# Kernel optimization log

Hardware: AMD Instinct MI355X
Metric: run time of the kernel (lower is better)

## Reference

```python
import jax, jax.numpy as jnp
import numpy as np

N, E, F_IN, D, L = 100000, 1600000, 32, 128, 5
B, V, T, EMB = 3000, 64, 128, 64
H = L * D  # 640 LSTM hidden
BN_EPS = 1e-5


def setup_inputs():
    key = jax.random.key(0)
    ks = jax.random.split(key, 20)
    rn = lambda k, s, sc=0.05: jax.random.normal(k, s, jnp.float32) * sc
    inp = {
        'x': jax.random.normal(ks[0], (N, F_IN), jnp.float32),
        'edge_index': jax.random.randint(ks[1], (2, E), 0, N, jnp.int32),
        'batch': jnp.sort(jax.random.randint(ks[2], (N,), 0, B, jnp.int32)),
        'smi': jax.random.randint(ks[3], (B, T), 0, V, jnp.int32),
        'gin0_w1': rn(ks[4], (F_IN, D)), 'gin0_b1': jnp.zeros((D,), jnp.float32),
        'gin0_w2': rn(ks[5], (D, D)),    'gin0_b2': jnp.zeros((D,), jnp.float32),
        'ginr_w1': rn(ks[6], (L - 1, D, D)), 'ginr_b1': jnp.zeros((L - 1, D), jnp.float32),
        'ginr_w2': rn(ks[7], (L - 1, D, D)), 'ginr_b2': jnp.zeros((L - 1, D), jnp.float32),
        'bn_gamma': jnp.ones((L, D), jnp.float32), 'bn_beta': jnp.zeros((L, D), jnp.float32),
        'emb': rn(ks[8], (V, EMB), 0.1).at[0].set(0.0),  # padding_idx=0
        'w_ih': rn(ks[9], (4 * H, EMB), 0.04), 'w_hh': rn(ks[10], (4 * H, H), 0.04),
        'b_ih': jnp.zeros((4 * H,), jnp.float32), 'b_hh': jnp.zeros((4 * H,), jnp.float32),
        'g_w1': rn(ks[11], (L * D, 4 * D)), 'g_b1': jnp.zeros((4 * D,), jnp.float32),
        'g_bn_gamma': jnp.ones((4 * D,), jnp.float32), 'g_bn_beta': jnp.zeros((4 * D,), jnp.float32),
        'g_w2': rn(ks[12], (4 * D, 6 * D)),
    }
    return inp


def _bn(h, gamma, beta):
    # BatchNorm1d in training mode: biased batch statistics
    mu = h.mean(0)
    var = h.var(0)
    return (h - mu) * jax.lax.rsqrt(var + BN_EPS) * gamma + beta


def _gin_layer(h, src, dst, w1, b1, w2, b2, gamma, beta):
    # GINConv (eps=0): MLP(x + sum_{j->i} x_j), then ReLU, then BN
    agg = jax.ops.segment_sum(h[src], dst, num_segments=N)  # [N, d]
    z = h + agg
    z = jnp.maximum(z @ w1 + b1, 0.0) @ w2 + b2
    z = jnp.maximum(z, 0.0)
    return _bn(z, gamma, beta)


def _lstm_last(e, w_ih, w_hh, b_ih, b_hh):
    # e: [B, T, EMB] -> last hidden state [B, H]
    def step(carry, xt):
        h, c = carry
        gates = xt @ w_ih.T + b_ih + h @ w_hh.T + b_hh  # [B, 4H]
        i, f, g, o = jnp.split(gates, 4, axis=1)  # torch gate order i,f,g,o
        c = jax.nn.sigmoid(f) * c + jax.nn.sigmoid(i) * jnp.tanh(g)
        h = jax.nn.sigmoid(o) * jnp.tanh(c)
        return (h, c), None
    h0 = jnp.zeros((e.shape[0], H), e.dtype)
    (h, _), _ = jax.lax.scan(step, (h0, h0), e.transpose(1, 0, 2))
    return h


def reference(x, edge_index, batch, smi, gin0_w1, gin0_b1, gin0_w2, gin0_b2,
              ginr_w1, ginr_b1, ginr_w2, ginr_b2, bn_gamma, bn_beta, emb,
              w_ih, w_hh, b_ih, b_hh, g_w1, g_b1, g_bn_gamma, g_bn_beta, g_w2):
    src, dst = edge_index[0], edge_index[1]
    # --- GIN encoder with layer-wise global_add_pool ---
    h = _gin_layer(x, src, dst, gin0_w1, gin0_b1, gin0_w2, gin0_b2, bn_gamma[0], bn_beta[0])
    pools = [jax.ops.segment_sum(h, batch, num_segments=B)]
    for i in range(L - 1):
        h = _gin_layer(h, src, dst, ginr_w1[i], ginr_b1[i], ginr_w2[i], ginr_b2[i],
                       bn_gamma[i + 1], bn_beta[i + 1])
        pools.append(jax.ops.segment_sum(h, batch, num_segments=B))
    enc1 = jnp.concatenate(pools, axis=1)  # [B, L*D]
    # --- SMILES encoder: Embedding + LSTM, take output at last timestep ---
    enc2 = _lstm_last(emb[smi], w_ih, w_hh, b_ih, b_hh)  # [B, H] == [B, L*D]
    # --- shared projection head g, L2-normalized (F.normalize, eps=1e-12) ---
    def g_head(z):
        z1 = jnp.maximum(_bn(z @ g_w1 + g_b1, g_bn_gamma, g_bn_beta), 0.0)
        out = z1 @ g_w2
        nrm = jnp.maximum(jnp.linalg.norm(out, axis=1, keepdims=True), 1e-12)
        return out / nrm
    return (g_head(enc1), g_head(enc2))
```

## Files before the change

### kernel.cpp

```cpp
#include <hip/hip_runtime.h>

typedef __bf16 bf16x8 __attribute__((ext_vector_type(8)));
typedef float f32x4 __attribute__((ext_vector_type(4)));
typedef unsigned short ushort8 __attribute__((ext_vector_type(8)));

#define DEV static __device__ __forceinline__

DEV unsigned short f2bf(float f){
  unsigned int u = __builtin_bit_cast(unsigned int, f);
  u += 0x7fffu + ((u >> 16) & 1u);
  return (unsigned short)(u >> 16);
}
DEV float bf2f(unsigned short u){
  return __builtin_bit_cast(float, ((unsigned int)u) << 16);
}
DEV float sigf(float x){ return 1.0f/(1.0f + __expf(-x)); }

static constexpr int NN   = 100000;
static constexpr int NPAD = 100096;
static constexpr int NE   = 1600000;
static constexpr int NB   = 3000;
static constexpr int BPAD = 3072;
static constexpr int TT   = 128;
static constexpr int HID  = 640;
static constexpr int SCAN_B = 1024;
static constexpr int NBLK = (NN + SCAN_B - 1)/SCAN_B;

__global__ void cvt_k(const float* __restrict__ s, unsigned short* __restrict__ d, int n){
  int i = blockIdx.x*256 + threadIdx.x; if (i < n) d[i] = f2bf(s[i]);
}
__global__ void transpose_cvt_split_k(const float* __restrict__ s, unsigned short* __restrict__ dh,
                                      unsigned short* __restrict__ dl, int R, int C){
  int i = blockIdx.x*256 + threadIdx.x; if (i >= R*C) return;
  int r = i / C, c = i - r*C;
  float v = s[i];
  unsigned short hi = f2bf(v);
  dh[c*R + r] = hi;
  dl[c*R + r] = f2bf(v - bf2f(hi));
}
__global__ void wc2_build_k(const float* __restrict__ whh, const float* __restrict__ wih,
                            unsigned short* __restrict__ wc2){
  int i = blockIdx.x*256 + threadIdx.x; if (i >= 2560*704) return;
  int n2 = i / 704, k = i - n2*704;
  int jt = n2 >> 7, rem = n2 & 127;
  int hc = rem >> 6, gate = (rem >> 4) & 3, j15 = rem & 15;
  int n = gate*640 + jt*32 + hc*16 + j15;
  float v = (k < 640) ? whh[n*640 + k] : wih[n*64 + (k - 640)];
  wc2[i] = f2bf(v);
}
__global__ void add_k(const float* __restrict__ a, const float* __restrict__ b, float* __restrict__ o, int n){
  int i = blockIdx.x*256 + threadIdx.x; if (i < n) o[i] = a[i] + b[i];
}

__global__ __launch_bounds__(256) void deg_hist_k(const int* __restrict__ dsts, int* __restrict__ deg){
  int e = blockIdx.x*256 + threadIdx.x; if (e < NE) atomicAdd(&deg[dsts[e]], 1);
}
__global__ __launch_bounds__(256) void scan_bsum_k(const int* __restrict__ deg, int* __restrict__ bsum){
  __shared__ int red[4];
  int b = blockIdx.x, tid = threadIdx.x;
  int base = b*SCAN_B + tid*4;
  int s = 0;
  #pragma unroll
  for (int q = 0; q < 4; ++q){ int idx = base + q; s += (idx < NN) ? deg[idx] : 0; }
  #pragma unroll
  for (int m = 1; m < 64; m <<= 1) s += __shfl_xor(s, m);
  if ((tid & 63) == 0) red[tid >> 6] = s;
  __syncthreads();
  if (tid == 0) bsum[b] = red[0] + red[1] + red[2] + red[3];
}
__global__ void scan_off_k(int* __restrict__ bsum){
  if (threadIdx.x == 0){
    int run = 0;
    for (int i = 0; i < NBLK; ++i){ int t = bsum[i]; bsum[i] = run; run += t; }
  }
}
__global__ __launch_bounds__(256) void scan_write_k(const int* __restrict__ deg, const int* __restrict__ bsum,
                                                    int* __restrict__ rowptr, int* __restrict__ cursor){
  __shared__ int tsum[256];
  int b = blockIdx.x, tid = threadIdx.x;
  int base = b*SCAN_B + tid*4;
  int v[4]; int s = 0;
  #pragma unroll
  for (int q = 0; q < 4; ++q){ int idx = base + q; v[q] = (idx < NN) ? deg[idx] : 0; s += v[q]; }
  tsum[tid] = s;
  __syncthreads();
  for (int offt = 1; offt < 256; offt <<= 1){
    int y = (tid >= offt) ? tsum[tid - offt] : 0;
    __syncthreads();
    tsum[tid] += y;
    __syncthreads();
  }
  int run = bsum[b] + tsum[tid] - s;
  #pragma unroll
  for (int q = 0; q < 4; ++q){
    int idx = base + q;
    if (idx < NN){ rowptr[idx] = run; cursor[idx] = run; }
    run += v[q];
  }
  if (b == 0 && tid == 0) rowptr[NN] = NE;
}
__global__ __launch_bounds__(256) void csr_fill_k(const int* __restrict__ srcs, const int* __restrict__ dsts,
                                                  int* __restrict__ cursor, int* __restrict__ eidx){
  int e = blockIdx.x*256 + threadIdx.x; if (e >= NE) return;
  int d = dsts[e];
  int pos = atomicAdd(&cursor[d], 1);
  eidx[pos] = srcs[e];
}

__global__ __launch_bounds__(256) void gbound_k(const int* __restrict__ batch, int* __restrict__ gstart){
  int i = blockIdx.x*256 + threadIdx.x;
  if (i >= NN) return;
  int bi = batch[i];
  int bp = (i == 0) ? -1 : batch[i-1];
  for (int g = bp + 1; g <= bi; ++g) gstart[g] = i;
  if (i == NN-1){
    for (int g = bi + 1; g <= NB; ++g) gstart[g] = NN;
  }
}

__global__ __launch_bounds__(256) void agg128_k(const int* __restrict__ rowptr, const int* __restrict__ eidx,
    const float* __restrict__ H, float* __restrict__ Z){
  int wid = (blockIdx.x*256 + threadIdx.x) >> 6;
  if (wid >= NN) return;
  int lane = threadIdx.x & 63;
  const float2* Hp = (const float2*)H;
  int n0 = rowptr[wid], n1 = rowptr[wid+1];
  float2 acc = Hp[(size_t)wid*64 + lane];
  int i = n0;
  for (; i + 1 < n1; i += 2){
    int s0 = eidx[i], s1 = eidx[i+1];
    float2 v0 = Hp[(size_t)s0*64 + lane];
    float2 v1 = Hp[(size_t)s1*64 + lane];
    acc.x += v0.x + v1.x; acc.y += v0.y + v1.y;
  }
  if (i < n1){
    float2 v = Hp[(size_t)eidx[i]*64 + lane];
    acc.x += v.x; acc.y += v.y;
  }
  ((float2*)Z)[(size_t)wid*64 + lane] = acc;
}
__global__ __launch_bounds__(256) void agg32_k(const int* __restrict__ rowptr, const int* __restrict__ eidx,
    const float* __restrict__ X, float* __restrict__ Z){
  int r = (blockIdx.x*256 + threadIdx.x) >> 5;
  if (r >= NN) return;
  int l = threadIdx.x & 31;
  int n0 = rowptr[r], n1 = rowptr[r+1];
  float acc = X[(size_t)r*32 + l];
  int i = n0;
  for (; i + 1 < n1; i += 2){
    int s0 = eidx[i], s1 = eidx[i+1];
    acc += X[(size_t)s0*32 + l] + X[(size_t)s1*32 + l];
  }
  if (i < n1) acc += X[(size_t)eidx[i]*32 + l];
  Z[(size_t)r*32 + l] = acc;
}

template<int KIN>
__global__ __launch_bounds__(256) void gin_mlp_k(const float* __restrict__ Z,
    const unsigned short* __restrict__ W1h, const unsigned short* __restrict__ W1l,
    const unsigned short* __restrict__ W2h, const unsigned short* __restrict__ W2l,
    const float* __restrict__ b1, const float* __restrict__ b2,
    float* __restrict__ Y, float* __restrict__ stats)
{
  constexpr int SA = KIN + 8;
  __shared__ __align__(16) unsigned short Ah[128*136];
  __shared__ __align__(16) unsigned short Al[128*136];
  const int tid = threadIdx.x, lane = tid & 63, w = tid >> 6;
  const int row0 = blockIdx.x * 128;
  const int wr = (w >> 1)*64, wc0 = (w & 1)*64;
  const int l15 = lane & 15, lg = lane >> 4;

  constexpr int CH = KIN/8;
  #pragma unroll
  for (int i = 0; i < (128*CH)/256; ++i){
    int chunk = tid + 256*i;
    int row = chunk / CH, kc = (chunk - row*CH)*8;
    const float* sp = Z + (size_t)(row0 + row)*KIN + kc;
    float4 a0 = *(const float4*)sp;
    float4 a1 = *(const float4*)(sp + 4);
    float vv[8] = {a0.x,a0.y,a0.z,a0.w,a1.x,a1.y,a1.z,a1.w};
    ushort8 vh, vl;
    #pragma unroll
    for (int q=0;q<8;++q){ unsigned short h = f2bf(vv[q]); vh[q]=h; vl[q]=f2bf(vv[q]-bf2f(h)); }
    *(ushort8*)&Ah[row*SA + kc] = vh;
    *(ushort8*)&Al[row*SA + kc] = vl;
  }
  __syncthreads();

  f32x4 acc[4][4];
  #pragma unroll
  for (int i=0;i<4;++i)
    #pragma unroll
    for (int j=0;j<4;++j) acc[i][j] = (f32x4)(0.0f);

  #pragma unroll
  for (int k0 = 0; k0 < KIN; k0 += 32){
    bf16x8 ah[4], al[4], bh[4], bl[4];
    #pragma unroll
    for (int fa=0; fa<4; ++fa){
      ah[fa] = *(const bf16x8*)&Ah[(wr + fa*16 + l15)*SA + k0 + 8*lg];
      al[fa] = *(const bf16x8*)&Al[(wr + fa*16 + l15)*SA + k0 + 8*lg];
    }
    #pragma unroll
    for (int fb=0; fb<4; ++fb){
      bh[fb] = *(const bf16x8*)&W1h[(wc0 + fb*16 + l15)*KIN + k0 + 8*lg];
      bl[fb] = *(const bf16x8*)&W1l[(wc0 + fb*16 + l15)*KIN + k0 + 8*lg];
    }
    #pragma unroll
    for (int fa=0; fa<4; ++fa)
      #pragma unroll
      for (int fb=0; fb<4; ++fb){
        acc[fa][fb] = __builtin_amdgcn_mfma_f32_16x16x32_bf16(ah[fa], bh[fb], acc[fa][fb], 0, 0, 0);
        acc[fa][fb] = __builtin_amdgcn_mfma_f32_16x16x32_bf16(al[fa], bh[fb], acc[fa][fb], 0, 0, 0);
        acc[fa][fb] = __builtin_amdgcn_mfma_f32_16x16x32_bf16(ah[fa], bl[fb], acc[fa][fb], 0, 0, 0);
      }
  }
  __syncthreads();

  {
    float b1v[4];
    #pragma unroll
    for (int fb=0; fb<4; ++fb) b1v[fb] = b1[wc0 + fb*16 + l15];
    #pragma unroll
    for (int fa=0; fa<4; ++fa)
      #pragma unroll
      for (int fb=0; fb<4; ++fb)
        #pragma unroll
        for (int r=0; r<4; ++r){
          float v = fmaxf(acc[fa][fb][r] + b1v[fb], 0.0f);
          unsigned short h = f2bf(v);
          int idx = (wr + fa*16 + lg*4 + r)*136 + (wc0 + fb*16 + l15);
          Ah[idx] = h;
          Al[idx] = f2bf(v - bf2f(h));
        }
  }
  __syncthreads();

  f32x4 acc2[4][4];
  #pragma unroll
  for (int i=0;i<4;++i)
    #pragma unroll
    for (int j=0;j<4;++j) acc2[i][j] = (f32x4)(0.0f);

  #pragma unroll
  for (int k0 = 0; k0 < 128; k0 += 32){
    bf16x8 ah[4], al[4], bh[4], bl[4];
    #pragma unroll
    for (int fa=0; fa<4; ++fa){
      ah[fa] = *(const bf16x8*)&Ah[(wr + fa*16 + l15)*136 + k0 + 8*lg];
      al[fa] = *(const bf16x8*)&Al[(wr + fa*16 + l15)*136 + k0 + 8*lg];
    }
    #pragma unroll
    for (int fb=0; fb<4; ++fb){
      bh[fb] = *(const bf16x8*)&W2h[(wc0 + fb*16 + l15)*128 + k0 + 8*lg];
      bl[fb] = *(const bf16x8*)&W2l[(wc0 + fb*16 + l15)*128 + k0 + 8*lg];
    }
    #pragma unroll
    for (int fa=0; fa<4; ++fa)
      #pragma unroll
      for (int fb=0; fb<4; ++fb){
        acc2[fa][fb] = __builtin_amdgcn_mfma_f32_16x16x32_bf16(ah[fa], bh[fb], acc2[fa][fb], 0, 0, 0);
        acc2[fa][fb] = __builtin_amdgcn_mfma_f32_16x16x32_bf16(al[fa], bh[fb], acc2[fa][fb], 0, 0, 0);
        acc2[fa][fb] = __builtin_amdgcn_mfma_f32_16x16x32_bf16(ah[fa], bl[fb], acc2[fa][fb], 0, 0, 0);
      }
  }

  float b2v[4]; int cc[4];
  #pragma unroll
  for (int fb=0; fb<4; ++fb){ cc[fb] = wc0 + fb*16 + l15; b2v[fb] = b2[cc[fb]]; }
  float ps[4] = {0,0,0,0}, pq[4] = {0,0,0,0};
  #pragma unroll
  for (int fa=0; fa<4; ++fa)
    #pragma unroll
    for (int fb=0; fb<4; ++fb)
      #pragma unroll
      for (int r=0; r<4; ++r){
        int row = row0 + wr + fa*16 + lg*4 + r;
        float v = fmaxf(acc2[fa][fb][r] + b2v[fb], 0.0f);
        if (row < NN){
          Y[(size_t)row*128 + cc[fb]] = v;
          ps[fb] += v; pq[fb] += v*v;
        }
      }
  #pragma unroll
  for (int fb=0; fb<4; ++fb){
    float s = ps[fb]; s += __shfl_xor(s, 16); s += __shfl_xor(s, 32);
    float q = pq[fb]; q += __shfl_xor(q, 16); q += __shfl_xor(q, 32);
    if (lane < 16){ atomicAdd(&stats[cc[fb]], s); atomicAdd(&stats[128 + cc[fb]], q); }
  }
}

__global__ void bn_finalize_k(const float* __restrict__ stats, const float* __restrict__ gamma,
                              const float* __restrict__ beta, float* __restrict__ sshift, int C, float invN){
  int c = blockIdx.x*blockDim.x + threadIdx.x; if (c >= C) return;
  float mean = stats[c]*invN;
  float var  = fmaxf(stats[C+c]*invN - mean*mean, 0.0f);
  float inv  = rsqrtf(var + 1e-5f);
  float sc   = gamma[c]*inv;
  sshift[c] = sc; sshift[C+c] = beta[c] - mean*sc;
}

__global__ __launch_bounds__(256) void bn_apply_k(const float* __restrict__ Y,
    const float* __restrict__ sshift, float* __restrict__ Hb)
{
  int gid = blockIdx.x*256 + threadIdx.x;
  int r = gid >> 5;
  if (r >= NN) return;
  int c0 = (gid & 31) << 2;
  float4 y = *(const float4*)&Y[(size_t)r*128 + c0];
  float4 h;
  h.x = y.x*sshift[c0+0] + sshift[128+c0+0];
  h.y = y.y*sshift[c0+1] + sshift[128+c0+1];
  h.z = y.z*sshift[c0+2] + sshift[128+c0+2];
  h.w = y.w*sshift[c0+3] + sshift[128+c0+3];
  *(float4*)&Hb[(size_t)r*128 + c0] = h;
}

__global__ __launch_bounds__(256) void pool_seg_k(const float* __restrict__ Hb,
    const int* __restrict__ gstart, float* __restrict__ pool, int layer)
{
  int g = blockIdx.x*4 + (threadIdx.x >> 6);
  if (g >= NB) return;
  int lane = threadIdx.x & 63;
  int n0 = gstart[g], n1 = gstart[g+1];
  const float2* Hp = (const float2*)Hb;
  float2 acc = make_float2(0.f, 0.f);
  for (int r = n0; r < n1; ++r){
    float2 v = Hp[(size_t)r*64 + lane];
    acc.x += v.x; acc.y += v.y;
  }
  ((float2*)pool)[(size_t)g*320 + layer*64 + lane] = acc;
}

__global__ __launch_bounds__(256) void embed_k(const int* __restrict__ smi,
    const unsigned short* __restrict__ emb_bf, unsigned short* __restrict__ e2){
  int gid = blockIdx.x*256 + threadIdx.x;
  int tb = gid >> 4;
  if (tb >= TT*BPAD) return;
  int t = tb / BPAD, b = tb - t*BPAD;
  int k4 = (gid & 15) << 2;
  uint2 v = make_uint2(0u, 0u);
  if (b < NB){
    int tok = smi[b*TT + t];
    v = *(const uint2*)&emb_bf[tok*64 + k4];
  }
  *(uint2*)&e2[(size_t)tb*64 + k4] = v;
}

__global__ __launch_bounds__(256) void lstm_step_k(const unsigned short* __restrict__ hprev,
    unsigned short* __restrict__ hnext, float* __restrict__ cbuf,
    const unsigned short* __restrict__ e2, const unsigned short* __restrict__ Wc2,
    const float* __restrict__ biasc, int t, float* __restrict__ hfin)
{
  __shared__ __align__(16) unsigned short As[2][128*40];
  __shared__ __align__(16) unsigned short Bs[2][128*40];
  const int tid = threadIdx.x, lane = tid & 63, w = tid >> 6;
  const int row0 = blockIdx.x * 128;
  const int jt = blockIdx.y;
  const int l15 = lane & 15, lg = lane >> 4;
  const int wr = (w >> 1)*64, wc0 = (w & 1)*64;

  const int srow = tid >> 2, skc = (tid & 3) << 3;
  const unsigned short* A0 = hprev + (size_t)(row0 + srow)*HID;
  const unsigned short* A1 = hprev + (size_t)(row0 + srow + 64)*HID;
  const unsigned short* E0 = e2 + ((size_t)t*BPAD + row0 + srow)*64;
  const unsigned short* E1 = e2 + ((size_t)t*BPAD + row0 + srow + 64)*64;
  const unsigned short* B0 = Wc2 + (size_t)(jt*128 + srow)*704;
  const unsigned short* B1 = Wc2 + (size_t)(jt*128 + srow + 64)*704;

  *(ushort8*)&As[0][srow*40 + skc]      = *(const ushort8*)&A0[skc];
  *(ushort8*)&As[0][(srow+64)*40 + skc] = *(const ushort8*)&A1[skc];
  *(ushort8*)&Bs[0][srow*40 + skc]      = *(const ushort8*)&B0[skc];
  *(ushort8*)&Bs[0][(srow+64)*40 + skc] = *(const ushort8*)&B1[skc];
  __syncthreads();

  f32x4 acc[4][4];
  #pragma unroll
  for (int i=0;i<4;++i)
    #pragma unroll
    for (int j=0;j<4;++j) acc[i][j] = (f32x4)(0.0f);

  int p = 0;
  for (int kk = 0; kk < 22; ++kk){
    ushort8 va0, va1, vb0, vb1;
    const int k1 = (kk+1)*32;
    if (kk < 21){
      if (k1 < 640){
        va0 = *(const ushort8*)&A0[k1 + skc];
        va1 = *(const ushort8*)&A1[k1 + skc];
      } else {
        va0 = *(const ushort8*)&E0[k1 - 640 + skc];
        va1 = *(const ushort8*)&E1[k1 - 640 + skc];
      }
      vb0 = *(const ushort8*)&B0[k1 + skc];
      vb1 = *(const ushort8*)&B1[k1 + skc];
    }
    bf16x8 a[4], b[4];
    #pragma unroll
    for (int fa=0; fa<4; ++fa) a[fa] = *(const bf16x8*)&As[p][(wr + fa*16 + l15)*40 + 8*lg];
    #pragma unroll
    for (int fb=0; fb<4; ++fb) b[fb] = *(const bf16x8*)&Bs[p][(wc0 + fb*16 + l15)*40 + 8*lg];
    #pragma unroll
    for (int fa=0; fa<4; ++fa)
      #pragma unroll
      for (int fb=0; fb<4; ++fb)
        acc[fa][fb] = __builtin_amdgcn_mfma_f32_16x16x32_bf16(a[fa], b[fb], acc[fa][fb], 0, 0, 0);
    if (kk < 21){
      *(ushort8*)&As[p^1][srow*40 + skc]      = va0;
      *(ushort8*)&As[p^1][(srow+64)*40 + skc] = va1;
      *(ushort8*)&Bs[p^1][srow*40 + skc]      = vb0;
      *(ushort8*)&Bs[p^1][(srow+64)*40 + skc] = vb1;
    }
    __syncthreads();
    p ^= 1;
  }

  const int j = jt*32 + (w & 1)*16 + l15;
  float bi = biasc[j], bf_ = biasc[640+j], bg = biasc[1280+j], bo = biasc[1920+j];
  #pragma unroll
  for (int fa=0; fa<4; ++fa){
    #pragma unroll
    for (int r=0; r<4; ++r){
      int br = row0 + wr + fa*16 + lg*4 + r;
      float iv = acc[fa][0][r] + bi;
      float fv = acc[fa][1][r] + bf_;
      float gv = acc[fa][2][r] + bg;
      float ov = acc[fa][3][r] + bo;
      size_t idx = (size_t)br*HID + j;
      float co = cbuf[idx];
      float cn = sigf(fv)*co + sigf(iv)*tanhf(gv);
      cbuf[idx] = cn;
      float hv = sigf(ov)*tanhf(cn);
      hnext[idx] = f2bf(hv);
      if (hfin) hfin[idx] = hv;
    }
  }
}

template<int DO_STATS>
__global__ __launch_bounds__(256) void gemm_split_k(const float* __restrict__ A,
    const unsigned short* __restrict__ Bh, const unsigned short* __restrict__ Bl,
    const float* __restrict__ bias, float* __restrict__ outp, float* __restrict__ stats,
    int Mvalid, int Nc, int K)
{
  __shared__ __align__(16) unsigned short Ah[128*40];
  __shared__ __align__(16) unsigned short Al[128*40];
  const int tid = threadIdx.x, lane = tid & 63, w = tid >> 6;
  const int row0 = blockIdx.x * 128, col0 = blockIdx.y * 128;
  const int wr = (w >> 1)*64, wc0 = (w & 1)*64;
  const int l15 = lane & 15, lg = lane >> 4;

  f32x4 acc[4][4];
  #pragma unroll
  for (int i=0;i<4;++i)
    #pragma unroll
    for (int j=0;j<4;++j) acc[i][j] = (f32x4)(0.0f);

  for (int k0 = 0; k0 < K; k0 += 32){
    #pragma unroll
    for (int i=0;i<2;++i){
      int chunk = tid + 256*i;
      int row = chunk >> 2, kc = (chunk & 3) << 3;
      const float* sp = A + (size_t)(row0+row)*K + k0 + kc;
      float4 a0 = *(const float4*)sp;
      float4 a1 = *(const float4*)(sp + 4);
      float vv[8] = {a0.x,a0.y,a0.z,a0.w,a1.x,a1.y,a1.z,a1.w};
      ushort8 vh, vl;
      #pragma unroll
      for (int q=0;q<8;++q){ unsigned short h = f2bf(vv[q]); vh[q]=h; vl[q]=f2bf(vv[q]-bf2f(h)); }
      *(ushort8*)&Ah[row*40 + kc] = vh;
      *(ushort8*)&Al[row*40 + kc] = vl;
    }
    __syncthreads();
    bf16x8 ah[4], al[4], bh[4], bl[4];
    #pragma unroll
    for (int fa=0; fa<4; ++fa){
      ah[fa] = *(const bf16x8*)&Ah[(wr + fa*16 + l15)*40 + 8*lg];
      al[fa] = *(const bf16x8*)&Al[(wr + fa*16 + l15)*40 + 8*lg];
    }
    #pragma unroll
    for (int fb=0; fb<4; ++fb){
      bh[fb] = *(const bf16x8*)&Bh[(size_t)(col0 + wc0 + fb*16 + l15)*K + k0 + 8*lg];
      bl[fb] = *(const bf16x8*)&Bl[(size_t)(col0 + wc0 + fb*16 + l15)*K + k0 + 8*lg];
    }
    #pragma unroll
    for (int fa=0; fa<4; ++fa)
      #pragma unroll
      for (int fb=0; fb<4; ++fb){
        acc[fa][fb] = __builtin_amdgcn_mfma_f32_16x16x32_bf16(ah[fa], bh[fb], acc[fa][fb], 0, 0, 0);
        acc[fa][fb] = __builtin_amdgcn_mfma_f32_16x16x32_bf16(al[fa], bh[fb], acc[fa][fb], 0, 0, 0);
        acc[fa][fb] = __builtin_amdgcn_mfma_f32_16x16x32_bf16(ah[fa], bl[fb], acc[fa][fb], 0, 0, 0);
      }
    __syncthreads();
  }

  float bv[4]; int cc[4];
  #pragma unroll
  for (int fb=0; fb<4; ++fb){ cc[fb] = col0 + wc0 + fb*16 + l15; bv[fb] = bias ? bias[cc[fb]] : 0.0f; }
  float ps[4] = {0,0,0,0}, pq[4] = {0,0,0,0};
  #pragma unroll
  for (int fa=0; fa<4; ++fa)
    #pragma unroll
    for (int fb=0; fb<4; ++fb)
      #pragma unroll
      for (int r=0; r<4; ++r){
        int row = row0 + wr + fa*16 + lg*4 + r;
        float v = acc[fa][fb][r] + bv[fb];
        if (row < Mvalid){
          outp[(size_t)row*Nc + cc[fb]] = v;
          if (DO_STATS){ ps[fb] += v; pq[fb] += v*v; }
        }
      }
  if (DO_STATS){
    #pragma unroll
    for (int fb=0; fb<4; ++fb){
      float s = ps[fb]; s += __shfl_xor(s, 16); s += __shfl_xor(s, 32);
      float q = pq[fb]; q += __shfl_xor(q, 16); q += __shfl_xor(q, 32);
      if (lane < 16){ atomicAdd(&stats[cc[fb]], s); atomicAdd(&stats[Nc + cc[fb]], q); }
    }
  }
}

__global__ __launch_bounds__(256) void bn_apply_head_k(const float* __restrict__ Zpre,
    const float* __restrict__ sshift, float* __restrict__ z1f){
  int gid = blockIdx.x*256 + threadIdx.x;
  int r = gid >> 7;
  if (r >= BPAD) return;
  int c0 = (gid & 127) << 2;
  float4 o = make_float4(0.f,0.f,0.f,0.f);
  if (r < NB){
    float4 v = *(const float4*)&Zpre[(size_t)r*512 + c0];
    o.x = fmaxf(v.x*sshift[c0+0] + sshift[512+c0+0], 0.0f);
    o.y = fmaxf(v.y*sshift[c0+1] + sshift[512+c0+1], 0.0f);
    o.z = fmaxf(v.z*sshift[c0+2] + sshift[512+c0+2], 0.0f);
    o.w = fmaxf(v.w*sshift[c0+3] + sshift[512+c0+3], 0.0f);
  }
  *(float4*)&z1f[(size_t)r*512 + c0] = o;
}

__global__ __launch_bounds__(256) void rownorm_k(const float* __restrict__ in, float* __restrict__ outp){
  int r = blockIdx.x;
  const float* p = in + (size_t)r*768;
  float ss = 0.0f;
  #pragma unroll
  for (int i = 0; i < 3; ++i){ float v = p[threadIdx.x + 256*i]; ss += v*v; }
  #pragma unroll
  for (int m = 1; m < 64; m <<= 1) ss += __shfl_xor(ss, m);
  __shared__ float red[4];
  if ((threadIdx.x & 63) == 0) red[threadIdx.x >> 6] = ss;
  __syncthreads();
  float tot = red[0] + red[1] + red[2] + red[3];
  float inv = 1.0f / fmaxf(sqrtf(tot), 1e-12f);
  float* q = outp + (size_t)r*768;
  #pragma unroll
  for (int i = 0; i < 3; ++i) q[threadIdx.x + 256*i] = p[threadIdx.x + 256*i]*inv;
}

static inline int cdiv(long a, long b){ return (int)((a + b - 1)/b); }

extern "C" void kernel_launch(void* const* d_in, const int* in_sizes, int n_in,
                              void* d_out, int out_size, void* d_ws, size_t ws_size,
                              hipStream_t stream)
{
  const float* x        = (const float*)d_in[0];
  const int*   edges    = (const int*)d_in[1];
  const int*   batch    = (const int*)d_in[2];
  const int*   smi      = (const int*)d_in[3];
  const float* gin0_w1  = (const float*)d_in[4];
  const float* gin0_b1  = (const float*)d_in[5];
  const float* gin0_w2  = (const float*)d_in[6];
  const float* gin0_b2  = (const float*)d_in[7];
  const float* ginr_w1  = (const float*)d_in[8];
  const float* ginr_b1  = (const float*)d_in[9];
  const float* ginr_w2  = (const float*)d_in[10];
  const float* ginr_b2  = (const float*)d_in[11];
  const float* bn_gamma = (const float*)d_in[12];
  const float* bn_beta  = (const float*)d_in[13];
  const float* emb      = (const float*)d_in[14];
  const float* w_ih     = (const float*)d_in[15];
  const float* w_hh     = (const float*)d_in[16];
  const float* b_ih     = (const float*)d_in[17];
  const float* b_hh     = (const float*)d_in[18];
  const float* g_w1     = (const float*)d_in[19];
  const float* g_b1     = (const float*)d_in[20];
  const float* g_bng    = (const float*)d_in[21];
  const float* g_bnb    = (const float*)d_in[22];
  const float* g_w2     = (const float*)d_in[23];
  float* outp = (float*)d_out;
  const int* srcs = edges;
  const int* dsts = edges + NE;

  char* base = (char*)d_ws;
  size_t off = 0;
  auto carve = [&](size_t bytes)->char*{ char* p = base + off; off += (bytes + 255) & ~(size_t)255; return p; };
  float* z_gin = (float*)carve((size_t)NPAD*128*4);
  float* y_gin = (float*)carve((size_t)NPAD*128*4);
  float* h_gin = (float*)carve((size_t)NPAD*128*4);
  float* pool  = (float*)carve((size_t)BPAD*HID*4);
  unsigned short* Wc2    = (unsigned short*)carve((size_t)2560*704*2);
  float*          biasc  = (float*)carve(2560*4);
  unsigned short* emb_bf = (unsigned short*)carve(4096*2);
  unsigned short* w1t0h  = (unsigned short*)carve(128*32*2);
  unsigned short* w1t0l  = (unsigned short*)carve(128*32*2);
  unsigned short* w2t0h  = (unsigned short*)carve(128*128*2);
  unsigned short* w2t0l  = (unsigned short*)carve(128*128*2);
  unsigned short* w1trh  = (unsigned short*)carve(4*16384*2);
  unsigned short* w1trl  = (unsigned short*)carve(4*16384*2);
  unsigned short* w2trh  = (unsigned short*)carve(4*16384*2);
  unsigned short* w2trl  = (unsigned short*)carve(4*16384*2);
  unsigned short* gw1th  = (unsigned short*)carve(512*640*2);
  unsigned short* gw1tl  = (unsigned short*)carve(512*640*2);
  unsigned short* gw2th  = (unsigned short*)carve(768*512*2);
  unsigned short* gw2tl  = (unsigned short*)carve(768*512*2);
  float* stats  = (float*)carve(1024*4);
  float* sshift = (float*)carve(1024*4);
  int* deg    = (int*)carve((size_t)NN*4);
  int* cursor = (int*)carve((size_t)NN*4);
  int* rowptr = (int*)carve((size_t)(NN+1)*4);
  int* bsum   = (int*)carve(512);
  int* eidx   = (int*)carve((size_t)NE*4);
  int* gstart = (int*)carve((size_t)(NB+1)*4);

  unsigned short* e2     = (unsigned short*)y_gin;
  unsigned short* h_a    = (unsigned short*)h_gin;
  unsigned short* h_b    = h_a + (size_t)BPAD*HID;
  float*          c_buf  = (float*)(h_b + (size_t)BPAD*HID);
  float*          hfin   = c_buf + (size_t)BPAD*HID;
  float*          z1pre  = (float*)z_gin;
  float*          z1f    = z1pre + (size_t)BPAD*512;
  float*          outtmp = z1f + (size_t)BPAD*512;

  wc2_build_k<<<cdiv((long)2560*704,256),256,0,stream>>>(w_hh, w_ih, Wc2);
  add_k<<<cdiv(2560,256),256,0,stream>>>(b_ih, b_hh, biasc, 2560);
  cvt_k<<<cdiv(4096,256),256,0,stream>>>(emb, emb_bf, 4096);
  transpose_cvt_split_k<<<cdiv(32*128,256),256,0,stream>>>(gin0_w1, w1t0h, w1t0l, 32, 128);
  transpose_cvt_split_k<<<cdiv(16384,256),256,0,stream>>>(gin0_w2, w2t0h, w2t0l, 128, 128);
  for (int i = 0; i < 4; ++i){
    transpose_cvt_split_k<<<cdiv(16384,256),256,0,stream>>>(ginr_w1 + (size_t)i*16384, w1trh + (size_t)i*16384, w1trl + (size_t)i*16384, 128, 128);
    transpose_cvt_split_k<<<cdiv(16384,256),256,0,stream>>>(ginr_w2 + (size_t)i*16384, w2trh + (size_t)i*16384, w2trl + (size_t)i*16384, 128, 128);
  }
  transpose_cvt_split_k<<<cdiv(640*512,256),256,0,stream>>>(g_w1, gw1th, gw1tl, 640, 512);
  transpose_cvt_split_k<<<cdiv(512*768,256),256,0,stream>>>(g_w2, gw2th, gw2tl, 512, 768);

  hipMemsetAsync(deg, 0, (size_t)NN*4, stream);
  deg_hist_k<<<cdiv(NE,256),256,0,stream>>>(dsts, deg);
  scan_bsum_k<<<NBLK,256,0,stream>>>(deg, bsum);
  scan_off_k<<<1,64,0,stream>>>(bsum);
  scan_write_k<<<NBLK,256,0,stream>>>(deg, bsum, rowptr, cursor);
  csr_fill_k<<<cdiv(NE,256),256,0,stream>>>(srcs, dsts, cursor, eidx);
  gbound_k<<<cdiv(NN,256),256,0,stream>>>(batch, gstart);

  for (int l = 0; l < 5; ++l){
    hipMemsetAsync(stats, 0, 1024*4, stream);
    if (l == 0)
      agg32_k<<<cdiv((long)NN*32,256),256,0,stream>>>(rowptr, eidx, x, z_gin);
    else
      agg128_k<<<cdiv((long)NN*64,256),256,0,stream>>>(rowptr, eidx, h_gin, z_gin);
    if (l == 0)
      gin_mlp_k<32><<<NPAD/128,256,0,stream>>>(z_gin, w1t0h, w1t0l, w2t0h, w2t0l, gin0_b1, gin0_b2, y_gin, stats);
    else
      gin_mlp_k<128><<<NPAD/128,256,0,stream>>>(z_gin, w1trh + (size_t)(l-1)*16384, w1trl + (size_t)(l-1)*16384,
                                                w2trh + (size_t)(l-1)*16384, w2trl + (size_t)(l-1)*16384,
                                                ginr_b1 + (l-1)*128, ginr_b2 + (l-1)*128, y_gin, stats);
    bn_finalize_k<<<1,128,0,stream>>>(stats, bn_gamma + l*128, bn_beta + l*128, sshift, 128, 1.0f/NN);
    bn_apply_k<<<cdiv((long)NN*32,256),256,0,stream>>>(y_gin, sshift, h_gin);
    pool_seg_k<<<cdiv(NB,4),256,0,stream>>>(h_gin, gstart, pool, l);
  }

  embed_k<<<cdiv((long)TT*BPAD*16,256),256,0,stream>>>(smi, emb_bf, e2);
  hipMemsetAsync(h_a, 0, (size_t)BPAD*HID*2, stream);
  hipMemsetAsync(c_buf, 0, (size_t)BPAD*HID*4, stream);
  for (int t = 0; t < TT; ++t){
    const unsigned short* hin = (t & 1) ? h_b : h_a;
    unsigned short* hout      = (t & 1) ? h_a : h_b;
    lstm_step_k<<<dim3(BPAD/128, 20),256,0,stream>>>(hin, hout, c_buf, e2, Wc2, biasc, t,
                                                     (t == TT-1) ? hfin : nullptr);
  }

  const float* headAf[2] = { pool, hfin };
  for (int hd = 0; hd < 2; ++hd){
    hipMemsetAsync(stats, 0, 1024*4, stream);
    gemm_split_k<1><<<dim3(BPAD/128, 4),256,0,stream>>>(headAf[hd], gw1th, gw1tl, g_b1, z1pre, stats, NB, 512, 640);
    bn_finalize_k<<<2,256,0,stream>>>(stats, g_bng, g_bnb, sshift, 512, 1.0f/NB);
    bn_apply_head_k<<<cdiv((long)BPAD*128,256),256,0,stream>>>(z1pre, sshift, z1f);
    gemm_split_k<0><<<dim3(BPAD/128, 6),256,0,stream>>>(z1f, gw2th, gw2tl, nullptr, outtmp, nullptr, NB, 768, 512);
    rownorm_k<<<NB,256,0,stream>>>(outtmp, outp + (size_t)hd*NB*768);
  }
}
```

Before: 4.749 ms.

## Fuse BN apply with pooling, fast tanh and MFMA priority in LSTM step

Merges the BatchNorm apply kernel and the per-graph pooling kernel into one pass that normalizes, writes h and accumulates the pool, removing one read of the node features and one launch per layer. The LSTM step swaps library tanhf for an exp-based approximation and raises wave priority around the MFMA block. The fused kernel only touches nodes covered by graph segments, and the fast tanh slightly changes numerics.

```diff
diff --git a/kernel.cpp b/kernel.cpp
--- a/kernel.cpp
+++ b/kernel.cpp
@@ -15,6 +15,12 @@
   return __builtin_bit_cast(float, ((unsigned int)u) << 16);
 }
 DEV float sigf(float x){ return 1.0f/(1.0f + __expf(-x)); }
+DEV float tanhf_fast(float x){
+  float ax = fabsf(x);
+  float e = __expf(2.0f*ax);
+  float r = 1.0f - 2.0f/(e + 1.0f);
+  return copysignf(r, x);
+}
 
 static constexpr int NN   = 100000;
 static constexpr int NPAD = 100096;
@@ -300,34 +306,25 @@
   sshift[c] = sc; sshift[C+c] = beta[c] - mean*sc;
 }
 
-__global__ __launch_bounds__(256) void bn_apply_k(const float* __restrict__ Y,
-    const float* __restrict__ sshift, float* __restrict__ Hb)
-{
-  int gid = blockIdx.x*256 + threadIdx.x;
-  int r = gid >> 5;
-  if (r >= NN) return;
-  int c0 = (gid & 31) << 2;
-  float4 y = *(const float4*)&Y[(size_t)r*128 + c0];
-  float4 h;
-  h.x = y.x*sshift[c0+0] + sshift[128+c0+0];
-  h.y = y.y*sshift[c0+1] + sshift[128+c0+1];
-  h.z = y.z*sshift[c0+2] + sshift[128+c0+2];
-  h.w = y.w*sshift[c0+3] + sshift[128+c0+3];
-  *(float4*)&Hb[(size_t)r*128 + c0] = h;
-}
-
-__global__ __launch_bounds__(256) void pool_seg_k(const float* __restrict__ Hb,
-    const int* __restrict__ gstart, float* __restrict__ pool, int layer)
+__global__ __launch_bounds__(256) void bn_pool_k(const float* __restrict__ Y,
+    const float* __restrict__ sshift, const int* __restrict__ gstart,
+    float* __restrict__ Hb, float* __restrict__ pool, int layer)
 {
   int g = blockIdx.x*4 + (threadIdx.x >> 6);
   if (g >= NB) return;
   int lane = threadIdx.x & 63;
+  int c0 = lane << 1;
+  float sc0 = sshift[c0],     sc1 = sshift[c0+1];
+  float sh0 = sshift[128+c0], sh1 = sshift[128+c0+1];
   int n0 = gstart[g], n1 = gstart[g+1];
-  const float2* Hp = (const float2*)Hb;
+  const float2* Yp = (const float2*)Y;
+  float2* Hp = (float2*)Hb;
   float2 acc = make_float2(0.f, 0.f);
   for (int r = n0; r < n1; ++r){
-    float2 v = Hp[(size_t)r*64 + lane];
-    acc.x += v.x; acc.y += v.y;
+    float2 y = Yp[(size_t)r*64 + lane];
+    float2 h = make_float2(y.x*sc0 + sh0, y.y*sc1 + sh1);
+    Hp[(size_t)r*64 + lane] = h;
+    acc.x += h.x; acc.y += h.y;
   }
   ((float2*)pool)[(size_t)g*320 + layer*64 + lane] = acc;
 }
@@ -400,11 +397,13 @@
     for (int fa=0; fa<4; ++fa) a[fa] = *(const bf16x8*)&As[p][(wr + fa*16 + l15)*40 + 8*lg];
     #pragma unroll
     for (int fb=0; fb<4; ++fb) b[fb] = *(const bf16x8*)&Bs[p][(wc0 + fb*16 + l15)*40 + 8*lg];
+    __builtin_amdgcn_s_setprio(1);
     #pragma unroll
     for (int fa=0; fa<4; ++fa)
       #pragma unroll
       for (int fb=0; fb<4; ++fb)
         acc[fa][fb] = __builtin_amdgcn_mfma_f32_16x16x32_bf16(a[fa], b[fb], acc[fa][fb], 0, 0, 0);
+    __builtin_amdgcn_s_setprio(0);
     if (kk < 21){
       *(ushort8*)&As[p^1][srow*40 + skc]      = va0;
       *(ushort8*)&As[p^1][(srow+64)*40 + skc] = va1;
@@ -428,9 +427,9 @@
       float ov = acc[fa][3][r] + bo;
       size_t idx = (size_t)br*HID + j;
       float co = cbuf[idx];
-      float cn = sigf(fv)*co + sigf(iv)*tanhf(gv);
+      float cn = sigf(fv)*co + sigf(iv)*tanhf_fast(gv);
       cbuf[idx] = cn;
-      float hv = sigf(ov)*tanhf(cn);
+      float hv = sigf(ov)*tanhf_fast(cn);
       hnext[idx] = f2bf(hv);
       if (hfin) hfin[idx] = hv;
     }
@@ -663,8 +662,7 @@
                                                 w2trh + (size_t)(l-1)*16384, w2trl + (size_t)(l-1)*16384,
                                                 ginr_b1 + (l-1)*128, ginr_b2 + (l-1)*128, y_gin, stats);
     bn_finalize_k<<<1,128,0,stream>>>(stats, bn_gamma + l*128, bn_beta + l*128, sshift, 128, 1.0f/NN);
-    bn_apply_k<<<cdiv((long)NN*32,256),256,0,stream>>>(y_gin, sshift, h_gin);
-    pool_seg_k<<<cdiv(NB,4),256,0,stream>>>(h_gin, gstart, pool, l);
+    bn_pool_k<<<cdiv(NB,4),256,0,stream>>>(y_gin, sshift, gstart, h_gin, pool, l);
   }
 
   embed_k<<<cdiv((long)TT*BPAD*16,256),256,0,stream>>>(smi, emb_bf, e2);
```

New measurement: 4.373 ms. 7.9% less time.
